# Optimization experiments

Hardware: AMD Instinct MI355X
Metric: run time of the kernel (lower is better)

Reference implementation:

```python
import jax, jax.numpy as jnp
import numpy as np

IN_FEATURES = 128
OUT_FEATURES = 32
N_NODES = 2048
ALPHA = 0.2  # LeakyReLU negative slope
NEG_INF = -9e15


def setup_inputs() -> dict:
    key = jax.random.key(0)
    k1, k2, k3, k4 = jax.random.split(key, 4)
    h = jax.random.normal(k1, (N_NODES, IN_FEATURES), dtype=jnp.float32)
    adj = jax.random.randint(k2, (N_NODES, N_NODES), 0, 2, dtype=jnp.int32)
    # xavier_uniform-ish scaling for params
    W = jax.random.normal(k3, (2 * IN_FEATURES, OUT_FEATURES), dtype=jnp.float32) * 0.1
    a = jax.random.normal(k4, (OUT_FEATURES,), dtype=jnp.float32) * 0.2
    return {"h": h, "adj": adj, "W": W, "a": a}


def reference(h, adj, W, a):
    in_f = h.shape[1]
    Wh1 = h @ W[:in_f, :]   # [N, F]
    Wh2 = h @ W[in_f:, :]   # [N, F]
    # GATv2 score: e[i,k] = sum_f a[f] * leaky_relu(Wh1[i,f] + Wh2[k,f])
    e = jax.nn.leaky_relu(Wh1[:, None, :] + Wh2[None, :, :], negative_slope=ALPHA)  # [N, N, F]
    e = jnp.einsum('ikf,f->ik', e, a)  # [N, N]
    att = jnp.where(adj > 0, e, NEG_INF)
    att = jax.nn.softmax(att, axis=1)
    h_prime = att @ Wh1  # note: original aggregates Wh1, faithful to source
    return jax.nn.elu(h_prime)  # concat=True -> ELU
```

## Files before the change

### kernel.cpp

```cpp
#include <hip/hip_runtime.h>
#include <math.h>

#define N_NODES 2048
#define IN_F 128
#define OUT_F 32
#define NEG_INF -9e15f
#define TI 8
#define NT 1024

__device__ __forceinline__ int pw(int k, int ih) {
    const int S = ((k >> 1) ^ (k >> 4)) & 7;
    return ((k << 3) | (ih << 2)) ^ (S << 2);
}

__global__ __launch_bounds__(256) void precompute_wh(
    const float* __restrict__ h, const float* __restrict__ W,
    const float* __restrict__ a,
    float* __restrict__ Wh1, float* __restrict__ Wh2T,
    float* __restrict__ Q, float* __restrict__ C)
{
    __shared__ float h_s[8][IN_F];
    __shared__ float tr[8][OUT_F];
    const int t = threadIdx.x;
    const int i0 = blockIdx.x * 8;

    ((float4*)&h_s[0][0])[t] = ((const float4*)(h + (size_t)i0 * IN_F))[t];
    __syncthreads();

    const int f = t & 31;
    const int r = t >> 5;
    float acc1 = 0.f, acc2 = 0.f;
    #pragma unroll 8
    for (int c = 0; c < IN_F; ++c) {
        const float hv = h_s[r][c];
        acc1 = fmaf(hv, W[c * OUT_F + f], acc1);
        acc2 = fmaf(hv, W[(IN_F + c) * OUT_F + f], acc2);
    }
    Wh1[(i0 + r) * OUT_F + f] = acc1;
    tr[r][f] = acc2;

    float q = 0.6f * a[f] * acc2;
    #pragma unroll
    for (int off = 16; off > 0; off >>= 1) q += __shfl_xor(q, off, 64);
    if (f == 0) Q[i0 + r] = q;
    if (blockIdx.x == 0 && t < OUT_F) C[t] = 0.4f * a[t];

    __syncthreads();
    const int f2 = t >> 3, r2 = t & 7;
    Wh2T[f2 * N_NODES + i0 + r2] = tr[r2][f2];
}

__global__ __launch_bounds__(NT) void gat_row(
    const float* __restrict__ Wh1, const float* __restrict__ Wh2T,
    const float* __restrict__ Q, const float* __restrict__ C,
    const int* __restrict__ adj, float* __restrict__ out)
{
    __shared__ __align__(16) float p_s[8 * (N_NODES / 2)];
    __shared__ __align__(16) float w1s[TI][OUT_F];
    __shared__ __align__(16) float part[16][TI][OUT_F];
    __shared__ float redM[TI][16], redL[TI][16], Mfin[TI];

    const int t = threadIdx.x;
    const int i0 = blockIdx.x * TI;
    const int k0 = 2 * t;
    const int lane = t & 63, wid = t >> 6;

    if (t < TI * OUT_F) w1s[t >> 5][t & 31] = Wh1[i0 * OUT_F + t];
    __syncthreads();

    int2 ad[TI];
    #pragma unroll
    for (int i = 0; i < TI; ++i)
        ad[i] = *(const int2*)(adj + (size_t)(i0 + i) * N_NODES + k0);
    const float2 q2 = *(const float2*)(Q + k0);

    float acc0[TI], acc1[TI];
    #pragma unroll
    for (int i = 0; i < TI; ++i) { acc0[i] = 0.f; acc1[i] = 0.f; }

    #pragma unroll 4
    for (int j = 0; j < 8; ++j) {
        float2 w2[4];
        #pragma unroll
        for (int e = 0; e < 4; ++e)
            w2[e] = *(const float2*)(Wh2T + (size_t)(4 * j + e) * N_NODES + k0);
        const float c0 = C[4 * j + 0], c1 = C[4 * j + 1];
        const float c2 = C[4 * j + 2], c3 = C[4 * j + 3];
        #pragma unroll
        for (int i = 0; i < TI; ++i) {
            const float4 w1 = *(const float4*)&w1s[i][4 * j];
            float x;
            x = w1.x + w2[0].x; acc0[i] = fmaf(c0, fabsf(x), acc0[i]);
            x = w1.x + w2[0].y; acc1[i] = fmaf(c0, fabsf(x), acc1[i]);
            x = w1.y + w2[1].x; acc0[i] = fmaf(c1, fabsf(x), acc0[i]);
            x = w1.y + w2[1].y; acc1[i] = fmaf(c1, fabsf(x), acc1[i]);
            x = w1.z + w2[2].x; acc0[i] = fmaf(c2, fabsf(x), acc0[i]);
            x = w1.z + w2[2].y; acc1[i] = fmaf(c2, fabsf(x), acc1[i]);
            x = w1.w + w2[3].x; acc0[i] = fmaf(c3, fabsf(x), acc0[i]);
            x = w1.w + w2[3].y; acc1[i] = fmaf(c3, fabsf(x), acc1[i]);
        }
    }

    #pragma unroll
    for (int i = 0; i < TI; ++i) {
        acc0[i] = (ad[i].x > 0) ? acc0[i] + q2.x : NEG_INF;
        acc1[i] = (ad[i].y > 0) ? acc1[i] + q2.y : NEG_INF;
        float mm = fmaxf(acc0[i], acc1[i]);
        #pragma unroll
        for (int off = 32; off > 0; off >>= 1)
            mm = fmaxf(mm, __shfl_xor(mm, off, 64));
        if (lane == 0) redM[i][wid] = mm;
    }
    __syncthreads();
    if (t < 128) {
        float v = redM[t >> 4][t & 15];
        #pragma unroll
        for (int off = 8; off > 0; off >>= 1)
            v = fmaxf(v, __shfl_xor(v, off, 64));
        if ((t & 15) == 0) Mfin[t >> 4] = v;
    }
    __syncthreads();

    float pr0[TI], pr1[TI];
    #pragma unroll
    for (int i = 0; i < TI; ++i) {
        const float M = Mfin[i];
        pr0[i] = __expf(acc0[i] - M);
        pr1[i] = __expf(acc1[i] - M);
        float ll = pr0[i] + pr1[i];
        #pragma unroll
        for (int off = 32; off > 0; off >>= 1)
            ll += __shfl_xor(ll, off, 64);
        if (lane == 0) redL[i][wid] = ll;
    }

    const int fq = (t & 7) * 4;
    const int c  = t >> 3;
    float4 av[TI];
    #pragma unroll
    for (int i = 0; i < TI; ++i) av[i] = make_float4(0.f, 0.f, 0.f, 0.f);

    #pragma unroll
    for (int h = 0; h < 2; ++h) {
        __syncthreads();
        if ((t >> 9) == h) {
            const int kl = 2 * (t & 511);
            *(float4*)&p_s[pw(kl, 0)]     = make_float4(pr0[0], pr0[1], pr0[2], pr0[3]);
            *(float4*)&p_s[pw(kl, 1)]     = make_float4(pr0[4], pr0[5], pr0[6], pr0[7]);
            *(float4*)&p_s[pw(kl + 1, 0)] = make_float4(pr1[0], pr1[1], pr1[2], pr1[3]);
            *(float4*)&p_s[pw(kl + 1, 1)] = make_float4(pr1[4], pr1[5], pr1[6], pr1[7]);
        }
        __syncthreads();
        #pragma unroll
        for (int it = 0; it < 8; ++it) {
            const int kl = 8 * c + it;
            const int kg = h * (N_NODES / 2) + kl;
            const float4 w  = *(const float4*)(Wh1 + (size_t)kg * OUT_F + fq);
            const float4 pA = *(const float4*)&p_s[pw(kl, 0)];
            const float4 pB = *(const float4*)&p_s[pw(kl, 1)];
            #define ACC(ii, pv) \
                av[ii].x = fmaf(pv, w.x, av[ii].x); \
                av[ii].y = fmaf(pv, w.y, av[ii].y); \
                av[ii].z = fmaf(pv, w.z, av[ii].z); \
                av[ii].w = fmaf(pv, w.w, av[ii].w);
            ACC(0, pA.x) ACC(1, pA.y) ACC(2, pA.z) ACC(3, pA.w)
            ACC(4, pB.x) ACC(5, pB.y) ACC(6, pB.z) ACC(7, pB.w)
            #undef ACC
        }
    }

    #pragma unroll
    for (int off = 8; off <= 32; off <<= 1) {
        #pragma unroll
        for (int i = 0; i < TI; ++i) {
            av[i].x += __shfl_xor(av[i].x, off, 64);
            av[i].y += __shfl_xor(av[i].y, off, 64);
            av[i].z += __shfl_xor(av[i].z, off, 64);
            av[i].w += __shfl_xor(av[i].w, off, 64);
        }
    }
    if (lane < 8) {
        #pragma unroll
        for (int i = 0; i < TI; ++i)
            *(float4*)&part[wid][i][fq] = av[i];
    }
    __syncthreads();

    if (t < TI * OUT_F) {
        const int i = t >> 5, f = t & 31;
        float s = 0.f;
        #pragma unroll
        for (int w = 0; w < 16; ++w) s += part[w][i][f];
        float L = 0.f;
        #pragma unroll
        for (int w = 0; w < 16; ++w) L += redL[i][w];
        const float val = s / L;
        out[(i0 + i) * OUT_F + f] = (val > 0.f) ? val : (__expf(val) - 1.f);
    }
}

extern "C" void kernel_launch(void* const* d_in, const int* in_sizes, int n_in,
                              void* d_out, int out_size, void* d_ws, size_t ws_size,
                              hipStream_t stream) {
    const float* h   = (const float*)d_in[0];
    const int*   adj = (const int*)d_in[1];
    const float* W   = (const float*)d_in[2];
    const float* a   = (const float*)d_in[3];
    float* out = (float*)d_out;

    float* Wh1  = (float*)d_ws;
    float* Wh2T = Wh1 + N_NODES * OUT_F;
    float* Q    = Wh2T + N_NODES * OUT_F;
    float* C    = Q + N_NODES;

    precompute_wh<<<N_NODES / 8, 256, 0, stream>>>(h, W, a, Wh1, Wh2T, Q, C);
    gat_row<<<N_NODES / TI, NT, 0, stream>>>(Wh1, Wh2T, Q, C, adj, out);
}
```

Before: 101.1 us.

## Retile GAT row kernel to 4 rows per 512-thread block with prefetching

Each block of the attention kernel now handles 4 rows with 512 threads, and each thread covers 4 columns instead of 2. The probability buffer is written once with a new swizzle instead of in two halves, removing a sync round. Wh2T and Wh1 loads are double-buffered in registers, and the adj/Q loads are moved late in the score loop to overlap latency. The change trades less reuse of each Wh2T load across rows for four times as many blocks and better occupancy.

```diff
diff --git a/kernel.cpp b/kernel.cpp
--- a/kernel.cpp
+++ b/kernel.cpp
@@ -5,12 +5,9 @@
 #define IN_F 128
 #define OUT_F 32
 #define NEG_INF -9e15f
-#define TI 8
-#define NT 1024
-
-__device__ __forceinline__ int pw(int k, int ih) {
-    const int S = ((k >> 1) ^ (k >> 4)) & 7;
-    return ((k << 3) | (ih << 2)) ^ (S << 2);
+
+__device__ __forceinline__ int pwd(int k) {
+    return (k << 2) ^ ((((k >> 3) ^ (k >> 5)) & 7) << 2);
 }
 
 __global__ __launch_bounds__(256) void precompute_wh(
@@ -50,129 +47,150 @@
     Wh2T[f2 * N_NODES + i0 + r2] = tr[r2][f2];
 }
 
-__global__ __launch_bounds__(NT) void gat_row(
+__global__ __launch_bounds__(512, 4) void gat_row(
     const float* __restrict__ Wh1, const float* __restrict__ Wh2T,
     const float* __restrict__ Q, const float* __restrict__ C,
     const int* __restrict__ adj, float* __restrict__ out)
 {
-    __shared__ __align__(16) float p_s[8 * (N_NODES / 2)];
-    __shared__ __align__(16) float w1s[TI][OUT_F];
-    __shared__ __align__(16) float part[16][TI][OUT_F];
-    __shared__ float redM[TI][16], redL[TI][16], Mfin[TI];
+    __shared__ __align__(16) float p_s[4 * N_NODES];
+    __shared__ __align__(16) float w1s[4][OUT_F];
+    __shared__ __align__(16) float part[8][4][OUT_F];
+    __shared__ float redM[4][8], redL[4][8], Mfin[4];
 
     const int t = threadIdx.x;
-    const int i0 = blockIdx.x * TI;
-    const int k0 = 2 * t;
+    const int i0 = blockIdx.x * 4;
+    const int k0 = 4 * t;
     const int lane = t & 63, wid = t >> 6;
 
-    if (t < TI * OUT_F) w1s[t >> 5][t & 31] = Wh1[i0 * OUT_F + t];
-    __syncthreads();
-
-    int2 ad[TI];
-    #pragma unroll
-    for (int i = 0; i < TI; ++i)
-        ad[i] = *(const int2*)(adj + (size_t)(i0 + i) * N_NODES + k0);
-    const float2 q2 = *(const float2*)(Q + k0);
-
-    float acc0[TI], acc1[TI];
-    #pragma unroll
-    for (int i = 0; i < TI; ++i) { acc0[i] = 0.f; acc1[i] = 0.f; }
-
-    #pragma unroll 4
-    for (int j = 0; j < 8; ++j) {
-        float2 w2[4];
-        #pragma unroll
-        for (int e = 0; e < 4; ++e)
-            w2[e] = *(const float2*)(Wh2T + (size_t)(4 * j + e) * N_NODES + k0);
-        const float c0 = C[4 * j + 0], c1 = C[4 * j + 1];
-        const float c2 = C[4 * j + 2], c3 = C[4 * j + 3];
-        #pragma unroll
-        for (int i = 0; i < TI; ++i) {
-            const float4 w1 = *(const float4*)&w1s[i][4 * j];
-            float x;
-            x = w1.x + w2[0].x; acc0[i] = fmaf(c0, fabsf(x), acc0[i]);
-            x = w1.x + w2[0].y; acc1[i] = fmaf(c0, fabsf(x), acc1[i]);
-            x = w1.y + w2[1].x; acc0[i] = fmaf(c1, fabsf(x), acc0[i]);
-            x = w1.y + w2[1].y; acc1[i] = fmaf(c1, fabsf(x), acc1[i]);
-            x = w1.z + w2[2].x; acc0[i] = fmaf(c2, fabsf(x), acc0[i]);
-            x = w1.z + w2[2].y; acc1[i] = fmaf(c2, fabsf(x), acc1[i]);
-            x = w1.w + w2[3].x; acc0[i] = fmaf(c3, fabsf(x), acc0[i]);
-            x = w1.w + w2[3].y; acc1[i] = fmaf(c3, fabsf(x), acc1[i]);
-        }
-    }
-
-    #pragma unroll
-    for (int i = 0; i < TI; ++i) {
-        acc0[i] = (ad[i].x > 0) ? acc0[i] + q2.x : NEG_INF;
-        acc1[i] = (ad[i].y > 0) ? acc1[i] + q2.y : NEG_INF;
-        float mm = fmaxf(acc0[i], acc1[i]);
+    if (t < 4 * OUT_F) w1s[t >> 5][t & 31] = Wh1[i0 * OUT_F + t];
+    __syncthreads();
+
+    float acc[4][4];
+    #pragma unroll
+    for (int i = 0; i < 4; ++i)
+        #pragma unroll
+        for (int c = 0; c < 4; ++c) acc[i][c] = 0.f;
+
+    float4 buf[2][4];
+    #pragma unroll
+    for (int e = 0; e < 4; ++e)
+        buf[0][e] = *(const float4*)(Wh2T + (size_t)e * N_NODES + k0);
+
+    int4 ad[4];
+    float4 q4;
+    #pragma unroll
+    for (int g = 0; g < 8; ++g) {
+        if (g < 7) {
+            #pragma unroll
+            for (int e = 0; e < 4; ++e)
+                buf[(g + 1) & 1][e] =
+                    *(const float4*)(Wh2T + (size_t)((g + 1) * 4 + e) * N_NODES + k0);
+        }
+        if (g == 6) {
+            #pragma unroll
+            for (int i = 0; i < 4; ++i)
+                ad[i] = *(const int4*)(adj + (size_t)(i0 + i) * N_NODES + k0);
+            q4 = *(const float4*)(Q + k0);
+        }
+        #pragma unroll
+        for (int i = 0; i < 4; ++i) {
+            const float4 w1 = *(const float4*)&w1s[i][4 * g];
+            #pragma unroll
+            for (int e = 0; e < 4; ++e) {
+                const float cf = C[4 * g + e];
+                const float4 w2 = buf[g & 1][e];
+                const float w1c = (e == 0) ? w1.x : (e == 1) ? w1.y
+                                 : (e == 2) ? w1.z : w1.w;
+                acc[i][0] = fmaf(cf, fabsf(w1c + w2.x), acc[i][0]);
+                acc[i][1] = fmaf(cf, fabsf(w1c + w2.y), acc[i][1]);
+                acc[i][2] = fmaf(cf, fabsf(w1c + w2.z), acc[i][2]);
+                acc[i][3] = fmaf(cf, fabsf(w1c + w2.w), acc[i][3]);
+            }
+        }
+    }
+
+    #pragma unroll
+    for (int i = 0; i < 4; ++i) {
+        acc[i][0] = (ad[i].x > 0) ? acc[i][0] + q4.x : NEG_INF;
+        acc[i][1] = (ad[i].y > 0) ? acc[i][1] + q4.y : NEG_INF;
+        acc[i][2] = (ad[i].z > 0) ? acc[i][2] + q4.z : NEG_INF;
+        acc[i][3] = (ad[i].w > 0) ? acc[i][3] + q4.w : NEG_INF;
+        float mm = fmaxf(fmaxf(acc[i][0], acc[i][1]), fmaxf(acc[i][2], acc[i][3]));
         #pragma unroll
         for (int off = 32; off > 0; off >>= 1)
             mm = fmaxf(mm, __shfl_xor(mm, off, 64));
         if (lane == 0) redM[i][wid] = mm;
     }
     __syncthreads();
-    if (t < 128) {
-        float v = redM[t >> 4][t & 15];
-        #pragma unroll
-        for (int off = 8; off > 0; off >>= 1)
+    if (t < 32) {
+        float v = redM[t >> 3][t & 7];
+        #pragma unroll
+        for (int off = 4; off > 0; off >>= 1)
             v = fmaxf(v, __shfl_xor(v, off, 64));
-        if ((t & 15) == 0) Mfin[t >> 4] = v;
-    }
-    __syncthreads();
-
-    float pr0[TI], pr1[TI];
-    #pragma unroll
-    for (int i = 0; i < TI; ++i) {
+        if ((t & 7) == 0) Mfin[t >> 3] = v;
+    }
+    __syncthreads();
+
+    float pr[4][4];
+    #pragma unroll
+    for (int i = 0; i < 4; ++i) {
         const float M = Mfin[i];
-        pr0[i] = __expf(acc0[i] - M);
-        pr1[i] = __expf(acc1[i] - M);
-        float ll = pr0[i] + pr1[i];
+        float ll = 0.f;
+        #pragma unroll
+        for (int c = 0; c < 4; ++c) {
+            pr[i][c] = __expf(acc[i][c] - M);
+            ll += pr[i][c];
+        }
         #pragma unroll
         for (int off = 32; off > 0; off >>= 1)
             ll += __shfl_xor(ll, off, 64);
         if (lane == 0) redL[i][wid] = ll;
     }
+    #pragma unroll
+    for (int kk = 0; kk < 4; ++kk)
+        *(float4*)&p_s[pwd(k0 + kk)] =
+            make_float4(pr[0][kk], pr[1][kk], pr[2][kk], pr[3][kk]);
+    __syncthreads();
 
     const int fq = (t & 7) * 4;
     const int c  = t >> 3;
-    float4 av[TI];
-    #pragma unroll
-    for (int i = 0; i < TI; ++i) av[i] = make_float4(0.f, 0.f, 0.f, 0.f);
-
-    #pragma unroll
-    for (int h = 0; h < 2; ++h) {
-        __syncthreads();
-        if ((t >> 9) == h) {
-            const int kl = 2 * (t & 511);
-            *(float4*)&p_s[pw(kl, 0)]     = make_float4(pr0[0], pr0[1], pr0[2], pr0[3]);
-            *(float4*)&p_s[pw(kl, 1)]     = make_float4(pr0[4], pr0[5], pr0[6], pr0[7]);
-            *(float4*)&p_s[pw(kl + 1, 0)] = make_float4(pr1[0], pr1[1], pr1[2], pr1[3]);
-            *(float4*)&p_s[pw(kl + 1, 1)] = make_float4(pr1[4], pr1[5], pr1[6], pr1[7]);
-        }
-        __syncthreads();
-        #pragma unroll
-        for (int it = 0; it < 8; ++it) {
-            const int kl = 8 * c + it;
-            const int kg = h * (N_NODES / 2) + kl;
-            const float4 w  = *(const float4*)(Wh1 + (size_t)kg * OUT_F + fq);
-            const float4 pA = *(const float4*)&p_s[pw(kl, 0)];
-            const float4 pB = *(const float4*)&p_s[pw(kl, 1)];
-            #define ACC(ii, pv) \
-                av[ii].x = fmaf(pv, w.x, av[ii].x); \
-                av[ii].y = fmaf(pv, w.y, av[ii].y); \
-                av[ii].z = fmaf(pv, w.z, av[ii].z); \
-                av[ii].w = fmaf(pv, w.w, av[ii].w);
-            ACC(0, pA.x) ACC(1, pA.y) ACC(2, pA.z) ACC(3, pA.w)
-            ACC(4, pB.x) ACC(5, pB.y) ACC(6, pB.z) ACC(7, pB.w)
-            #undef ACC
+    float4 av[4];
+    #pragma unroll
+    for (int i = 0; i < 4; ++i) av[i] = make_float4(0.f, 0.f, 0.f, 0.f);
+
+    float4 wbuf[2][4];
+    #pragma unroll
+    for (int e = 0; e < 4; ++e)
+        wbuf[0][e] = *(const float4*)(Wh1 + (size_t)(32 * c + e) * OUT_F + fq);
+
+    #pragma unroll
+    for (int kg = 0; kg < 8; ++kg) {
+        if (kg < 7) {
+            #pragma unroll
+            for (int e = 0; e < 4; ++e)
+                wbuf[(kg + 1) & 1][e] =
+                    *(const float4*)(Wh1 + (size_t)(32 * c + 4 * (kg + 1) + e) * OUT_F + fq);
+        }
+        #pragma unroll
+        for (int e = 0; e < 4; ++e) {
+            const int k = 32 * c + 4 * kg + e;
+            const float4 p = *(const float4*)&p_s[pwd(k)];
+            const float4 w = wbuf[kg & 1][e];
+            av[0].x = fmaf(p.x, w.x, av[0].x); av[0].y = fmaf(p.x, w.y, av[0].y);
+            av[0].z = fmaf(p.x, w.z, av[0].z); av[0].w = fmaf(p.x, w.w, av[0].w);
+            av[1].x = fmaf(p.y, w.x, av[1].x); av[1].y = fmaf(p.y, w.y, av[1].y);
+            av[1].z = fmaf(p.y, w.z, av[1].z); av[1].w = fmaf(p.y, w.w, av[1].w);
+            av[2].x = fmaf(p.z, w.x, av[2].x); av[2].y = fmaf(p.z, w.y, av[2].y);
+            av[2].z = fmaf(p.z, w.z, av[2].z); av[2].w = fmaf(p.z, w.w, av[2].w);
+            av[3].x = fmaf(p.w, w.x, av[3].x); av[3].y = fmaf(p.w, w.y, av[3].y);
+            av[3].z = fmaf(p.w, w.z, av[3].z); av[3].w = fmaf(p.w, w.w, av[3].w);
         }
     }
 
     #pragma unroll
     for (int off = 8; off <= 32; off <<= 1) {
         #pragma unroll
-        for (int i = 0; i < TI; ++i) {
+        for (int i = 0; i < 4; ++i) {
             av[i].x += __shfl_xor(av[i].x, off, 64);
             av[i].y += __shfl_xor(av[i].y, off, 64);
             av[i].z += __shfl_xor(av[i].z, off, 64);
@@ -181,19 +199,19 @@
     }
     if (lane < 8) {
         #pragma unroll
-        for (int i = 0; i < TI; ++i)
-            *(float4*)&part[wid][i][fq] = av[i];
-    }
-    __syncthreads();
-
-    if (t < TI * OUT_F) {
+        for (int i = 0; i < 4; ++i)
+            *(float4*)&part[wid][i][4 * lane] = av[i];
+    }
+    __syncthreads();
+
+    if (t < 4 * OUT_F) {
         const int i = t >> 5, f = t & 31;
         float s = 0.f;
         #pragma unroll
-        for (int w = 0; w < 16; ++w) s += part[w][i][f];
+        for (int w = 0; w < 8; ++w) s += part[w][i][f];
         float L = 0.f;
         #pragma unroll
-        for (int w = 0; w < 16; ++w) L += redL[i][w];
+        for (int w = 0; w < 8; ++w) L += redL[i][w];
         const float val = s / L;
         out[(i0 + i) * OUT_F + f] = (val > 0.f) ? val : (__expf(val) - 1.f);
     }
@@ -214,5 +232,5 @@
     float* C    = Q + N_NODES;
 
     precompute_wh<<<N_NODES / 8, 256, 0, stream>>>(h, W, a, Wh1, Wh2T, Q, C);
-    gat_row<<<N_NODES / TI, NT, 0, stream>>>(Wh1, Wh2T, Q, C, adj, out);
-}
+    gat_row<<<N_NODES / 4, 512, 0, stream>>>(Wh1, Wh2T, Q, C, adj, out);
+}
```

Result: slower. 165.7 us (+63.9%).

## Split attention rows across column chunks with flash-style partial softmax combine

Applied to the files above, without the earlier changes.

Replaces the 1024-thread per-row-block kernel with a split-K scheme. Each 64-thread block handles 8 rows by 128 columns, computes a local max, sum and weighted partial output, and writes them to workspace. A new combine kernel rescales and merges the 16 chunks, then applies the ELU. The goal is to drop the block-wide barriers and the large shared-memory buffer and to spread the work across many small blocks. In exchange it adds a third launch and extra workspace traffic for the partial results.

```diff
diff --git a/kernel.cpp b/kernel.cpp
--- a/kernel.cpp
+++ b/kernel.cpp
@@ -5,12 +5,12 @@
 #define IN_F 128
 #define OUT_F 32
 #define NEG_INF -9e15f
+#define KB 16
+#define KC 128
 #define TI 8
-#define NT 1024
-
-__device__ __forceinline__ int pw(int k, int ih) {
-    const int S = ((k >> 1) ^ (k >> 4)) & 7;
-    return ((k << 3) | (ih << 2)) ^ (S << 2);
+
+__device__ __forceinline__ int pcol(int k) {
+    return k ^ (((k >> 4) & 7) << 2);
 }
 
 __global__ __launch_bounds__(256) void precompute_wh(
@@ -50,122 +50,104 @@
     Wh2T[f2 * N_NODES + i0 + r2] = tr[r2][f2];
 }
 
-__global__ __launch_bounds__(NT) void gat_row(
+__global__ __launch_bounds__(64, 4) void gat_partial(
     const float* __restrict__ Wh1, const float* __restrict__ Wh2T,
     const float* __restrict__ Q, const float* __restrict__ C,
-    const int* __restrict__ adj, float* __restrict__ out)
+    const int* __restrict__ adj,
+    float* __restrict__ m_ws, float* __restrict__ l_ws,
+    float* __restrict__ o_ws)
 {
-    __shared__ __align__(16) float p_s[8 * (N_NODES / 2)];
     __shared__ __align__(16) float w1s[TI][OUT_F];
-    __shared__ __align__(16) float part[16][TI][OUT_F];
-    __shared__ float redM[TI][16], redL[TI][16], Mfin[TI];
-
-    const int t = threadIdx.x;
-    const int i0 = blockIdx.x * TI;
-    const int k0 = 2 * t;
-    const int lane = t & 63, wid = t >> 6;
-
-    if (t < TI * OUT_F) w1s[t >> 5][t & 31] = Wh1[i0 * OUT_F + t];
+    __shared__ __align__(16) float p_s[TI * KC];
+
+    const int lane = threadIdx.x;
+    const int ib = blockIdx.x >> 4;
+    const int cb = blockIdx.x & 15;
+    const int i0 = ib * TI;
+    const int kg = cb * KC + 2 * lane;
+
+    ((float4*)w1s)[lane] = ((const float4*)(Wh1 + (size_t)i0 * OUT_F))[lane];
     __syncthreads();
 
     int2 ad[TI];
     #pragma unroll
     for (int i = 0; i < TI; ++i)
-        ad[i] = *(const int2*)(adj + (size_t)(i0 + i) * N_NODES + k0);
-    const float2 q2 = *(const float2*)(Q + k0);
-
-    float acc0[TI], acc1[TI];
-    #pragma unroll
-    for (int i = 0; i < TI; ++i) { acc0[i] = 0.f; acc1[i] = 0.f; }
-
-    #pragma unroll 4
+        ad[i] = *(const int2*)(adj + (size_t)(i0 + i) * N_NODES + kg);
+    const float2 q2 = *(const float2*)(Q + kg);
+
+    float a0[TI], a1[TI];
+    #pragma unroll
+    for (int i = 0; i < TI; ++i) { a0[i] = 0.f; a1[i] = 0.f; }
+
+    #pragma unroll
     for (int j = 0; j < 8; ++j) {
         float2 w2[4];
         #pragma unroll
         for (int e = 0; e < 4; ++e)
-            w2[e] = *(const float2*)(Wh2T + (size_t)(4 * j + e) * N_NODES + k0);
+            w2[e] = *(const float2*)(Wh2T + (size_t)(4 * j + e) * N_NODES + kg);
         const float c0 = C[4 * j + 0], c1 = C[4 * j + 1];
         const float c2 = C[4 * j + 2], c3 = C[4 * j + 3];
         #pragma unroll
         for (int i = 0; i < TI; ++i) {
             const float4 w1 = *(const float4*)&w1s[i][4 * j];
             float x;
-            x = w1.x + w2[0].x; acc0[i] = fmaf(c0, fabsf(x), acc0[i]);
-            x = w1.x + w2[0].y; acc1[i] = fmaf(c0, fabsf(x), acc1[i]);
-            x = w1.y + w2[1].x; acc0[i] = fmaf(c1, fabsf(x), acc0[i]);
-            x = w1.y + w2[1].y; acc1[i] = fmaf(c1, fabsf(x), acc1[i]);
-            x = w1.z + w2[2].x; acc0[i] = fmaf(c2, fabsf(x), acc0[i]);
-            x = w1.z + w2[2].y; acc1[i] = fmaf(c2, fabsf(x), acc1[i]);
-            x = w1.w + w2[3].x; acc0[i] = fmaf(c3, fabsf(x), acc0[i]);
-            x = w1.w + w2[3].y; acc1[i] = fmaf(c3, fabsf(x), acc1[i]);
+            x = w1.x + w2[0].x; a0[i] = fmaf(c0, fabsf(x), a0[i]);
+            x = w1.x + w2[0].y; a1[i] = fmaf(c0, fabsf(x), a1[i]);
+            x = w1.y + w2[1].x; a0[i] = fmaf(c1, fabsf(x), a0[i]);
+            x = w1.y + w2[1].y; a1[i] = fmaf(c1, fabsf(x), a1[i]);
+            x = w1.z + w2[2].x; a0[i] = fmaf(c2, fabsf(x), a0[i]);
+            x = w1.z + w2[2].y; a1[i] = fmaf(c2, fabsf(x), a1[i]);
+            x = w1.w + w2[3].x; a0[i] = fmaf(c3, fabsf(x), a0[i]);
+            x = w1.w + w2[3].y; a1[i] = fmaf(c3, fabsf(x), a1[i]);
         }
     }
 
     #pragma unroll
     for (int i = 0; i < TI; ++i) {
-        acc0[i] = (ad[i].x > 0) ? acc0[i] + q2.x : NEG_INF;
-        acc1[i] = (ad[i].y > 0) ? acc1[i] + q2.y : NEG_INF;
-        float mm = fmaxf(acc0[i], acc1[i]);
+        const float s0 = (ad[i].x > 0) ? a0[i] + q2.x : NEG_INF;
+        const float s1 = (ad[i].y > 0) ? a1[i] + q2.y : NEG_INF;
+        float mm = fmaxf(s0, s1);
         #pragma unroll
         for (int off = 32; off > 0; off >>= 1)
             mm = fmaxf(mm, __shfl_xor(mm, off, 64));
-        if (lane == 0) redM[i][wid] = mm;
-    }
-    __syncthreads();
-    if (t < 128) {
-        float v = redM[t >> 4][t & 15];
-        #pragma unroll
-        for (int off = 8; off > 0; off >>= 1)
-            v = fmaxf(v, __shfl_xor(v, off, 64));
-        if ((t & 15) == 0) Mfin[t >> 4] = v;
-    }
-    __syncthreads();
-
-    float pr0[TI], pr1[TI];
-    #pragma unroll
-    for (int i = 0; i < TI; ++i) {
-        const float M = Mfin[i];
-        pr0[i] = __expf(acc0[i] - M);
-        pr1[i] = __expf(acc1[i] - M);
-        float ll = pr0[i] + pr1[i];
+        const float p0 = (s0 > 0.5f * NEG_INF) ? __expf(s0 - mm) : 0.f;
+        const float p1 = (s1 > 0.5f * NEG_INF) ? __expf(s1 - mm) : 0.f;
+        float ll = p0 + p1;
         #pragma unroll
         for (int off = 32; off > 0; off >>= 1)
             ll += __shfl_xor(ll, off, 64);
-        if (lane == 0) redL[i][wid] = ll;
-    }
-
-    const int fq = (t & 7) * 4;
-    const int c  = t >> 3;
+        *(float2*)&p_s[i * KC + pcol(2 * lane)] = make_float2(p0, p1);
+        if (lane == 0) {
+            m_ws[(size_t)(i0 + i) * KB + cb] = mm;
+            l_ws[(size_t)(i0 + i) * KB + cb] = ll;
+        }
+    }
+    __syncthreads();
+
+    const int fq = (lane & 7) * 4;
+    const int cp = lane >> 3;
     float4 av[TI];
     #pragma unroll
     for (int i = 0; i < TI; ++i) av[i] = make_float4(0.f, 0.f, 0.f, 0.f);
 
     #pragma unroll
-    for (int h = 0; h < 2; ++h) {
-        __syncthreads();
-        if ((t >> 9) == h) {
-            const int kl = 2 * (t & 511);
-            *(float4*)&p_s[pw(kl, 0)]     = make_float4(pr0[0], pr0[1], pr0[2], pr0[3]);
-            *(float4*)&p_s[pw(kl, 1)]     = make_float4(pr0[4], pr0[5], pr0[6], pr0[7]);
-            *(float4*)&p_s[pw(kl + 1, 0)] = make_float4(pr1[0], pr1[1], pr1[2], pr1[3]);
-            *(float4*)&p_s[pw(kl + 1, 1)] = make_float4(pr1[4], pr1[5], pr1[6], pr1[7]);
-        }
-        __syncthreads();
-        #pragma unroll
-        for (int it = 0; it < 8; ++it) {
-            const int kl = 8 * c + it;
-            const int kg = h * (N_NODES / 2) + kl;
-            const float4 w  = *(const float4*)(Wh1 + (size_t)kg * OUT_F + fq);
-            const float4 pA = *(const float4*)&p_s[pw(kl, 0)];
-            const float4 pB = *(const float4*)&p_s[pw(kl, 1)];
-            #define ACC(ii, pv) \
-                av[ii].x = fmaf(pv, w.x, av[ii].x); \
-                av[ii].y = fmaf(pv, w.y, av[ii].y); \
-                av[ii].z = fmaf(pv, w.z, av[ii].z); \
-                av[ii].w = fmaf(pv, w.w, av[ii].w);
-            ACC(0, pA.x) ACC(1, pA.y) ACC(2, pA.z) ACC(3, pA.w)
-            ACC(4, pB.x) ACC(5, pB.y) ACC(6, pB.z) ACC(7, pB.w)
-            #undef ACC
+    for (int g = 0; g < 4; ++g) {
+        const int kl = 16 * cp + 4 * g;
+        float4 w[4];
+        #pragma unroll
+        for (int d = 0; d < 4; ++d)
+            w[d] = *(const float4*)(Wh1 + (size_t)(cb * KC + kl + d) * OUT_F + fq);
+        #pragma unroll
+        for (int i = 0; i < TI; ++i) {
+            const float4 pv = *(const float4*)&p_s[i * KC + pcol(kl)];
+            av[i].x = fmaf(pv.x, w[0].x, av[i].x); av[i].y = fmaf(pv.x, w[0].y, av[i].y);
+            av[i].z = fmaf(pv.x, w[0].z, av[i].z); av[i].w = fmaf(pv.x, w[0].w, av[i].w);
+            av[i].x = fmaf(pv.y, w[1].x, av[i].x); av[i].y = fmaf(pv.y, w[1].y, av[i].y);
+            av[i].z = fmaf(pv.y, w[1].z, av[i].z); av[i].w = fmaf(pv.y, w[1].w, av[i].w);
+            av[i].x = fmaf(pv.z, w[2].x, av[i].x); av[i].y = fmaf(pv.z, w[2].y, av[i].y);
+            av[i].z = fmaf(pv.z, w[2].z, av[i].z); av[i].w = fmaf(pv.z, w[2].w, av[i].w);
+            av[i].x = fmaf(pv.w, w[3].x, av[i].x); av[i].y = fmaf(pv.w, w[3].y, av[i].y);
+            av[i].z = fmaf(pv.w, w[3].z, av[i].z); av[i].w = fmaf(pv.w, w[3].w, av[i].w);
         }
     }
 
@@ -182,21 +164,33 @@
     if (lane < 8) {
         #pragma unroll
         for (int i = 0; i < TI; ++i)
-            *(float4*)&part[wid][i][fq] = av[i];
-    }
-    __syncthreads();
-
-    if (t < TI * OUT_F) {
-        const int i = t >> 5, f = t & 31;
-        float s = 0.f;
-        #pragma unroll
-        for (int w = 0; w < 16; ++w) s += part[w][i][f];
-        float L = 0.f;
-        #pragma unroll
-        for (int w = 0; w < 16; ++w) L += redL[i][w];
-        const float val = s / L;
-        out[(i0 + i) * OUT_F + f] = (val > 0.f) ? val : (__expf(val) - 1.f);
-    }
+            *(float4*)&o_ws[((size_t)(i0 + i) * KB + cb) * OUT_F + fq] = av[i];
+    }
+}
+
+__global__ __launch_bounds__(256) void gat_combine(
+    const float* __restrict__ m_ws, const float* __restrict__ l_ws,
+    const float* __restrict__ o_ws, float* __restrict__ out)
+{
+    const int g = blockIdx.x * 256 + threadIdx.x;
+    const int i = g >> 5, f = g & 31;
+
+    float mv[KB];
+    float M = NEG_INF;
+    #pragma unroll
+    for (int c = 0; c < KB; ++c) {
+        mv[c] = m_ws[(size_t)i * KB + c];
+        M = fmaxf(M, mv[c]);
+    }
+    float L = 0.f, S = 0.f;
+    #pragma unroll
+    for (int c = 0; c < KB; ++c) {
+        const float wc = __expf(mv[c] - M);
+        L = fmaf(l_ws[(size_t)i * KB + c], wc, L);
+        S = fmaf(o_ws[((size_t)i * KB + c) * OUT_F + f], wc, S);
+    }
+    const float val = S / L;
+    out[g] = (val > 0.f) ? val : (__expf(val) - 1.f);
 }
 
 extern "C" void kernel_launch(void* const* d_in, const int* in_sizes, int n_in,
@@ -208,11 +202,17 @@
     const float* a   = (const float*)d_in[3];
     float* out = (float*)d_out;
 
-    float* Wh1  = (float*)d_ws;
+    float* ws   = (float*)d_ws;
+    float* Wh1  = ws;
     float* Wh2T = Wh1 + N_NODES * OUT_F;
     float* Q    = Wh2T + N_NODES * OUT_F;
     float* C    = Q + N_NODES;
+    float* m_ws = C + 64;
+    float* l_ws = m_ws + (size_t)N_NODES * KB;
+    float* o_ws = l_ws + (size_t)N_NODES * KB;
 
     precompute_wh<<<N_NODES / 8, 256, 0, stream>>>(h, W, a, Wh1, Wh2T, Q, C);
-    gat_row<<<N_NODES / TI, NT, 0, stream>>>(Wh1, Wh2T, Q, C, adj, out);
-}
+    gat_partial<<<(N_NODES / TI) * KB, 64, 0, stream>>>(Wh1, Wh2T, Q, C, adj,
+                                                        m_ws, l_ws, o_ws);
+    gat_combine<<<(N_NODES * OUT_F) / 256, 256, 0, stream>>>(m_ws, l_ws, o_ws, out);
+}
```

Result: slower. 186.7 us (+84.7%).
